# Kernel optimization log

Hardware: AMD Instinct MI355X
Metric: run time of the kernel (lower is better)

## Reference

```python
import math
import jax, jax.numpy as jnp
import numpy as np

NH, NKV, HD = 16, 8, 128  # n_heads, n_kv_heads, head_dim from config

def setup_inputs() -> dict:
    key = jax.random.key(0)
    ks = jax.random.split(key, 5)
    B, T, D = 2, 2048, 2048
    KV = NKV * HD  # 1024
    s = 1.0 / math.sqrt(D)
    return {
        "x": jax.random.normal(ks[0], (B, T, D), dtype=jnp.float32),
        "Wq": jax.random.normal(ks[1], (D, D), dtype=jnp.float32) * s,
        "Wk": jax.random.normal(ks[2], (KV, D), dtype=jnp.float32) * s,
        "Wv": jax.random.normal(ks[3], (KV, D), dtype=jnp.float32) * s,
        "Wo": jax.random.normal(ks[4], (D, D), dtype=jnp.float32) * s,
    }

def reference(x, Wq, Wk, Wv, Wo):
    B, T, D = x.shape
    groups = NH // NKV
    scale = 1.0 / math.sqrt(HD)
    # Projections (torch Linear: y = x @ W.T)
    q = (x @ Wq.T).reshape(B, T, NH, HD).transpose(0, 2, 1, 3)    # [B, nh, T, hd]
    k = (x @ Wk.T).reshape(B, T, NKV, HD).transpose(0, 2, 1, 3)   # [B, nkv, T, hd]
    v = (x @ Wv.T).reshape(B, T, NKV, HD).transpose(0, 2, 1, 3)   # [B, nkv, T, hd]
    kv_state = jnp.concatenate([k, v], axis=-1)                    # [B, nkv, T, 2*hd]
    # GQA: replicate kv heads (repeat_interleave along head dim)
    k = jnp.repeat(k, groups, axis=1)                              # [B, nh, T, hd]
    v = jnp.repeat(v, groups, axis=1)
    scores = jnp.einsum('bhqd,bhkd->bhqk', q, k) * scale           # [B, nh, T, T]
    causal = jnp.tril(jnp.ones((T, T), dtype=bool))
    scores = jnp.where(causal, scores, jnp.finfo(scores.dtype).min)
    probs = jax.nn.softmax(scores, axis=-1)
    attn = jnp.einsum('bhqk,bhkd->bhqd', probs, v)                 # [B, nh, T, hd]
    attn = attn.transpose(0, 2, 1, 3).reshape(B, T, NH * HD)
    output = attn @ Wo.T
    return (output, kv_state)
```

## Files before the change

### kernel.cpp

```cpp
#include <hip/hip_runtime.h>
#include <hip/hip_bf16.h>
#include <cstdint>
#include <cstddef>

#define DEV __device__ __forceinline__

typedef __attribute__((ext_vector_type(8))) short short8;
typedef __attribute__((ext_vector_type(4))) float f32x4;
typedef __attribute__((ext_vector_type(8))) __bf16 bf16x8;

DEV unsigned short f2bf(float f) {
    unsigned u = __builtin_bit_cast(unsigned, f);
    u += 0x7fffu + ((u >> 16) & 1u);
    return (unsigned short)(u >> 16);
}

DEV unsigned short f2bf_hw(float f) {
    return __builtin_bit_cast(unsigned short, (__bf16)f);
}

DEV f32x4 mfma16(short8 a, short8 b, f32x4 c) {
    return __builtin_amdgcn_mfma_f32_16x16x32_bf16(
        __builtin_bit_cast(bf16x8, a), __builtin_bit_cast(bf16x8, b), c, 0, 0, 0);
}

#define GLD_TO_LDS16(g, l)                                                  \
    __builtin_amdgcn_global_load_lds(                                       \
        (const __attribute__((address_space(1))) void*)(g),                 \
        (__attribute__((address_space(3))) void*)(l), 16, 0, 0)

__global__ void cvt_all(const float* __restrict__ x,  const float* __restrict__ wq,
                        const float* __restrict__ wk, const float* __restrict__ wv,
                        const float* __restrict__ wo,
                        unsigned short* __restrict__ xb,  unsigned short* __restrict__ wqb,
                        unsigned short* __restrict__ wkb, unsigned short* __restrict__ wvb,
                        unsigned short* __restrict__ wob) {
    constexpr int NX = 1048576, NQ = 524288, NK = 262144, NV = 262144, NO = 524288;
    constexpr int C1 = NX, C2 = C1 + NQ, C3 = C2 + NK, C4 = C3 + NV, C5 = C4 + NO;
    int i = blockIdx.x * blockDim.x + threadIdx.x;
    int stride = gridDim.x * blockDim.x;
    for (; i < C5; i += stride) {
        const float* s;
        unsigned short* d;
        int j;
        if (i < C1)      { s = x;  d = xb;  j = i; }
        else if (i < C2) { s = wq; d = wqb; j = i - C1; }
        else if (i < C3) { s = wk; d = wkb; j = i - C2; }
        else if (i < C4) { s = wv; d = wvb; j = i - C3; }
        else             { s = wo; d = wob; j = i - C4; }
        const f32x4* sp = (const f32x4*)(s + (size_t)j * 8);
        f32x4 a = sp[0], bq = sp[1];
        short8 o;
        o[0] = (short)f2bf(a[0]);  o[1] = (short)f2bf(a[1]);
        o[2] = (short)f2bf(a[2]);  o[3] = (short)f2bf(a[3]);
        o[4] = (short)f2bf(bq[0]); o[5] = (short)f2bf(bq[1]);
        o[6] = (short)f2bf(bq[2]); o[7] = (short)f2bf(bq[3]);
        *(short8*)(d + (size_t)j * 8) = o;
    }
}

__global__ __launch_bounds__(256) void transpose_v(
    const unsigned short* __restrict__ src, unsigned short* __restrict__ dst) {
    __shared__ __align__(16) unsigned short tile[64 * 64];
    const int t0 = blockIdx.x * 64;
    const int d0 = blockIdx.y * 64;
    const int b  = blockIdx.z;
    const int tid = threadIdx.x;
#pragma unroll
    for (int p = 0; p < 2; ++p) {
        int ch = tid + p * 256;
        int it = ch >> 3, ic8 = ch & 7;
        short8 v = *(const short8*)(src + (size_t)(b * 2048 + t0 + it) * 1024 + d0 + ic8 * 8);
        *(short8*)&tile[it * 64 + ((ic8 ^ (it & 7)) << 3)] = v;
    }
    __syncthreads();
#pragma unroll
    for (int p = 0; p < 2; ++p) {
        int ch = tid + p * 256;
        int od = ch >> 3, ot8 = ch & 7;
        short8 v;
#pragma unroll
        for (int j = 0; j < 8; ++j) {
            int t = ot8 * 8 + j;
            v[j] = (short)tile[t * 64 + ((((od >> 3) ^ (t & 7)) << 3) | (od & 7))];
        }
        *(short8*)(dst + (size_t)(b * 1024 + d0 + od) * 2048 + t0 + ot8 * 8) = v;
    }
}

__global__ __launch_bounds__(512, 2) void gemm_qkv_8p(
    const unsigned short* __restrict__ A,
    const unsigned short* __restrict__ Wq, const unsigned short* __restrict__ Wk,
    const unsigned short* __restrict__ Wv,
    unsigned short* __restrict__ Qo, unsigned short* __restrict__ Ko,
    unsigned short* __restrict__ Vo, float* __restrict__ kvf) {
    constexpr int K = 2048, BM = 256, KT = K / 64;
    __shared__ __align__(16) unsigned short sA[2][2][BM][32];
    __shared__ __align__(16) unsigned short sB[2][2][BM][32];

    const int tid = threadIdx.x, lane = tid & 63, w = tid >> 6;
    const int wm = w >> 2, wn = w & 3;
    const int lrow = lane & 15, lg = lane >> 4;
    const int m0 = blockIdx.y * BM, n0 = blockIdx.x * BM;

    const unsigned short* Bp;
    unsigned short* Co;
    int c0, ostr, doff = 0;
    bool iskv = false;
    if (n0 < 2048)      { Bp = Wq + (size_t)n0 * K;        Co = Qo; c0 = n0;        ostr = 2048; }
    else if (n0 < 3072) { Bp = Wk + (size_t)(n0-2048) * K; Co = Ko; c0 = n0 - 2048; ostr = 1024; iskv = true; }
    else                { Bp = Wv + (size_t)(n0-3072) * K; Co = Vo; c0 = n0 - 3072; ostr = 1024; iskv = true; doff = 128; }

    const unsigned short* Ab = A + (size_t)m0 * K;

    auto stage = [&](const unsigned short* gcol, unsigned short* lds) {
#pragma unroll
        for (int p = 0; p < 2; ++p) {
            int ch = tid + p * 512;
            int row = ch >> 2;
            int slot = (ch & 3) ^ (row & 3);
            GLD_TO_LDS16(gcol + (size_t)row * K + slot * 8, lds + ch * 8);
        }
    };

    f32x4 acc[8][4];
#pragma unroll
    for (int i = 0; i < 8; ++i)
#pragma unroll
        for (int j = 0; j < 4; ++j) acc[i][j] = (f32x4)0.f;

    const int xoff = (lg * 8) ^ ((lrow & 3) << 3);
    const int arow0 = wm * 128 + lrow;
    const int brow0 = wn * 64 + lrow;

    stage(Ab,      &sA[0][0][0][0]);
    stage(Bp,      &sB[0][0][0][0]);
    stage(Ab + 32, &sA[0][1][0][0]);
    stage(Bp + 32, &sB[0][1][0][0]);
    asm volatile("s_waitcnt vmcnt(4)\n\ts_barrier" ::: "memory");

    for (int kt = 0; kt < KT; ++kt) {
        const int buf = kt & 1, nb = buf ^ 1;
        const bool pre = (kt + 1 < KT);
        const unsigned short* An = Ab + (kt + 1) * 64;
        const unsigned short* Bn = Bp + (kt + 1) * 64;
        short8 bfrag[4], afrag[4];

        if (pre) stage(An, &sA[nb][0][0][0]);
#pragma unroll
        for (int ni = 0; ni < 4; ++ni)
            bfrag[ni] = *(const short8*)(&sB[buf][0][brow0 + ni * 16][0] + xoff);
#pragma unroll
        for (int mi = 0; mi < 4; ++mi)
            afrag[mi] = *(const short8*)(&sA[buf][0][arow0 + mi * 16][0] + xoff);
        __builtin_amdgcn_s_setprio(1);
#pragma unroll
        for (int mi = 0; mi < 4; ++mi)
#pragma unroll
            for (int ni = 0; ni < 4; ++ni)
                acc[mi][ni] = mfma16(afrag[mi], bfrag[ni], acc[mi][ni]);
        __builtin_amdgcn_s_setprio(0);

        if (pre) stage(Bn, &sB[nb][0][0][0]);
#pragma unroll
        for (int mi = 0; mi < 4; ++mi)
            afrag[mi] = *(const short8*)(&sA[buf][0][arow0 + 64 + mi * 16][0] + xoff);
        __builtin_amdgcn_s_setprio(1);
#pragma unroll
        for (int mi = 0; mi < 4; ++mi)
#pragma unroll
            for (int ni = 0; ni < 4; ++ni)
                acc[4 + mi][ni] = mfma16(afrag[mi], bfrag[ni], acc[4 + mi][ni]);
        __builtin_amdgcn_s_setprio(0);

        if (pre) asm volatile("s_waitcnt vmcnt(4)\n\ts_barrier" ::: "memory");
        else     asm volatile("s_waitcnt vmcnt(0)\n\ts_barrier" ::: "memory");

        if (pre) stage(An + 32, &sA[nb][1][0][0]);
#pragma unroll
        for (int ni = 0; ni < 4; ++ni)
            bfrag[ni] = *(const short8*)(&sB[buf][1][brow0 + ni * 16][0] + xoff);
#pragma unroll
        for (int mi = 0; mi < 4; ++mi)
            afrag[mi] = *(const short8*)(&sA[buf][1][arow0 + mi * 16][0] + xoff);
        __builtin_amdgcn_s_setprio(1);
#pragma unroll
        for (int mi = 0; mi < 4; ++mi)
#pragma unroll
            for (int ni = 0; ni < 4; ++ni)
                acc[mi][ni] = mfma16(afrag[mi], bfrag[ni], acc[mi][ni]);
        __builtin_amdgcn_s_setprio(0);

        if (pre) stage(Bn + 32, &sB[nb][1][0][0]);
#pragma unroll
        for (int mi = 0; mi < 4; ++mi)
            afrag[mi] = *(const short8*)(&sA[buf][1][arow0 + 64 + mi * 16][0] + xoff);
        __builtin_amdgcn_s_setprio(1);
#pragma unroll
        for (int mi = 0; mi < 4; ++mi)
#pragma unroll
            for (int ni = 0; ni < 4; ++ni)
                acc[4 + mi][ni] = mfma16(afrag[mi], bfrag[ni], acc[4 + mi][ni]);
        __builtin_amdgcn_s_setprio(0);

        if (pre) asm volatile("s_waitcnt vmcnt(4)\n\ts_barrier" ::: "memory");
    }

    const int lrow4 = (lane >> 4) * 4, lcol = lane & 15;
#pragma unroll
    for (int mi = 0; mi < 8; ++mi) {
#pragma unroll
        for (int ni = 0; ni < 4; ++ni) {
#pragma unroll
            for (int r = 0; r < 4; ++r) {
                int row = m0 + wm * 128 + mi * 16 + lrow4 + r;
                int col = c0 + wn * 64 + ni * 16 + lcol;
                float v = acc[mi][ni][r];
                Co[(size_t)row * ostr + col] = f2bf(v);
                if (iskv) {
                    int b = row >> 11, t = row & 2047;
                    int kh = col >> 7, d = col & 127;
                    kvf[((size_t)(b * 8 + kh) * 2048 + t) * 256 + doff + d] = v;
                }
            }
        }
    }
}

__global__ __launch_bounds__(512, 2) void gemm_o_2p(
    const unsigned short* __restrict__ A, const unsigned short* __restrict__ Bm,
    float* __restrict__ Cf) {
    constexpr int K = 2048, N = 2048, KT = K / 64;
    __shared__ __align__(16) unsigned short sA[2][2][256][32];
    __shared__ __align__(16) unsigned short sB[2][2][128][32];

    const int tid = threadIdx.x, lane = tid & 63, w = tid >> 6;
    const int wm = w >> 1, wn = w & 1;
    const int lrow = lane & 15, lg = lane >> 4;
    const int m0 = blockIdx.y * 256, n0 = blockIdx.x * 128;

    const unsigned short* Ab = A + (size_t)m0 * K;
    const unsigned short* Bb = Bm + (size_t)n0 * K;

    auto stageA = [&](const unsigned short* gcol, unsigned short* lds) {
#pragma unroll
        for (int p = 0; p < 2; ++p) {
            int ch = tid + p * 512;
            int row = ch >> 2;
            int slot = (ch & 3) ^ (row & 3);
            GLD_TO_LDS16(gcol + (size_t)row * K + slot * 8, lds + ch * 8);
        }
    };
    auto stageB = [&](const unsigned short* gcol, unsigned short* lds) {
        int ch = tid;
        int row = ch >> 2;
        int slot = (ch & 3) ^ (row & 3);
        GLD_TO_LDS16(gcol + (size_t)row * K + slot * 8, lds + ch * 8);
    };

    f32x4 acc[4][4];
#pragma unroll
    for (int i = 0; i < 4; ++i)
#pragma unroll
        for (int j = 0; j < 4; ++j) acc[i][j] = (f32x4)0.f;

    const int xoff = (lg * 8) ^ ((lrow & 3) << 3);
    const int arow0 = wm * 64 + lrow;
    const int brow0 = wn * 64 + lrow;

    stageA(Ab,      &sA[0][0][0][0]);
    stageB(Bb,      &sB[0][0][0][0]);
    stageA(Ab + 32, &sA[0][1][0][0]);
    stageB(Bb + 32, &sB[0][1][0][0]);
    asm volatile("s_waitcnt vmcnt(3)\n\ts_barrier" ::: "memory");

    for (int kt = 0; kt < KT; ++kt) {
        const int buf = kt & 1, nb = buf ^ 1;
        const bool pre = (kt + 1 < KT);
        const unsigned short* An = Ab + (kt + 1) * 64;
        const unsigned short* Bn = Bb + (kt + 1) * 64;
        short8 afrag[4], bfrag[4];

        if (pre) { stageA(An, &sA[nb][0][0][0]); stageB(Bn, &sB[nb][0][0][0]); }
#pragma unroll
        for (int ni = 0; ni < 4; ++ni)
            bfrag[ni] = *(const short8*)(&sB[buf][0][brow0 + ni * 16][0] + xoff);
#pragma unroll
        for (int mi = 0; mi < 4; ++mi)
            afrag[mi] = *(const short8*)(&sA[buf][0][arow0 + mi * 16][0] + xoff);
        __builtin_amdgcn_s_setprio(1);
#pragma unroll
        for (int mi = 0; mi < 4; ++mi)
#pragma unroll
            for (int ni = 0; ni < 4; ++ni)
                acc[mi][ni] = mfma16(afrag[mi], bfrag[ni], acc[mi][ni]);
        __builtin_amdgcn_s_setprio(0);

        if (pre) asm volatile("s_waitcnt vmcnt(3)\n\ts_barrier" ::: "memory");
        else     asm volatile("s_waitcnt vmcnt(0)\n\ts_barrier" ::: "memory");

        if (pre) { stageA(An + 32, &sA[nb][1][0][0]); stageB(Bn + 32, &sB[nb][1][0][0]); }
#pragma unroll
        for (int ni = 0; ni < 4; ++ni)
            bfrag[ni] = *(const short8*)(&sB[buf][1][brow0 + ni * 16][0] + xoff);
#pragma unroll
        for (int mi = 0; mi < 4; ++mi)
            afrag[mi] = *(const short8*)(&sA[buf][1][arow0 + mi * 16][0] + xoff);
        __builtin_amdgcn_s_setprio(1);
#pragma unroll
        for (int mi = 0; mi < 4; ++mi)
#pragma unroll
            for (int ni = 0; ni < 4; ++ni)
                acc[mi][ni] = mfma16(afrag[mi], bfrag[ni], acc[mi][ni]);
        __builtin_amdgcn_s_setprio(0);

        if (pre) asm volatile("s_waitcnt vmcnt(3)\n\ts_barrier" ::: "memory");
    }

    const int lrow4 = (lane >> 4) * 4, lcol = lane & 15;
#pragma unroll
    for (int mi = 0; mi < 4; ++mi)
#pragma unroll
        for (int ni = 0; ni < 4; ++ni)
#pragma unroll
            for (int r = 0; r < 4; ++r) {
                int row = m0 + wm * 64 + mi * 16 + lrow4 + r;
                int col = n0 + wn * 64 + ni * 16 + lcol;
                Cf[(size_t)row * N + col] = acc[mi][ni][r];
            }
}

__global__ __launch_bounds__(512, 2) void attn_fwd(
    const unsigned short* __restrict__ Qb, const unsigned short* __restrict__ Kb,
    const unsigned short* __restrict__ Vtg, unsigned short* __restrict__ Ob) {
    constexpr int T = 2048, DQ = 2048, DKV = 1024, HD = 128;
    constexpr float SC2 = 0.08838834764831845f * 1.4426950408889634f;
    constexpr float SHIFT = 8.0f * 1.4426950408889634f;
    __shared__ __align__(16) unsigned short Ks[2][64][128];
    __shared__ __align__(16) unsigned short Vs[2][128][64];
    __shared__ __align__(16) unsigned short Ps[8][16][64];

    const int bx = blockIdx.x, kh = blockIdx.y, b = blockIdx.z;
    const int qtile = b ? (31 - bx) : bx;
    const int tid = threadIdx.x, lane = tid & 63, w = tid >> 6;
    const int h = kh * 2 + (w >> 2);
    const int lrow = lane & 15, lg = lane >> 4;
    const int qt0 = qtile * 64;
    const int qrow0 = qt0 + (w & 3) * 16;
    const size_t bT = (size_t)b * T;

    short8 qf[4];
    {
        const unsigned short* qbase = Qb + (bT + qrow0 + lrow) * DQ + h * HD + lg * 8;
#pragma unroll
        for (int kc = 0; kc < 4; ++kc) qf[kc] = *(const short8*)(qbase + kc * 32);
    }

    int kr[2], kc8[2], vd[2], vk8[2];
#pragma unroll
    for (int p = 0; p < 2; ++p) {
        int ch = tid + p * 512;
        kr[p] = ch >> 4;  kc8[p] = ch & 15;
        vd[p] = ch >> 3;  vk8[p] = ch & 7;
    }
    const unsigned short* kbase = Kb + bT * DKV + kh * HD;
    const unsigned short* vbase = Vtg + (size_t)(b * 8 + kh) * 128 * T;
    short8 kreg[2], vreg[2];
    auto gload = [&](int kt) {
#pragma unroll
        for (int p = 0; p < 2; ++p) {
            kreg[p] = *(const short8*)(kbase + (size_t)(kt * 64 + kr[p]) * DKV + kc8[p] * 8);
            vreg[p] = *(const short8*)(vbase + (size_t)vd[p] * T + kt * 64 + vk8[p] * 8);
        }
    };
    auto lwrite = [&](int buf) {
#pragma unroll
        for (int p = 0; p < 2; ++p) {
            *(short8*)&Ks[buf][kr[p]][(kc8[p] ^ (kr[p] & 15)) << 3] = kreg[p];
            *(short8*)&Vs[buf][vd[p]][(vk8[p] ^ (vd[p] & 7)) << 3] = vreg[p];
        }
    };

    f32x4 o[8];
#pragma unroll
    for (int i = 0; i < 8; ++i) o[i] = (f32x4)0.f;
    float rsum[4] = {0.f, 0.f, 0.f, 0.f};

    const int nkt = qtile + 1;
    gload(0);
    for (int kt = 0; kt < nkt; ++kt) {
        const int kt0 = kt * 64;
        const int buf = kt & 1;
        lwrite(buf);
        __syncthreads();
        if (kt + 1 < nkt) gload(kt + 1);

        f32x4 s[4];
        __builtin_amdgcn_s_setprio(1);
#pragma unroll
        for (int nt = 0; nt < 4; ++nt) {
            s[nt] = (f32x4)0.f;
#pragma unroll
            for (int kc = 0; kc < 4; ++kc) {
                short8 kf = *(const short8*)&Ks[buf][nt * 16 + lrow][((kc * 4 + lg) ^ lrow) << 3];
                s[nt] = mfma16(qf[kc], kf, s[nt]);
            }
        }
        __builtin_amdgcn_s_setprio(0);

        const int qabs = qrow0 + lg * 4;
        const bool diag = (kt == qtile);
#pragma unroll
        for (int nt = 0; nt < 4; ++nt) {
            int kcol = kt0 + nt * 16 + lrow;
#pragma unroll
            for (int r = 0; r < 4; ++r) {
                float p = exp2f(fmaf(s[nt][r], SC2, -SHIFT));
                if (diag && kcol > qabs + r) p = 0.f;
                rsum[r] += p;
                int q = lg * 4 + r;
                Ps[w][q][((((nt * 2) + (lrow >> 3)) ^ (q & 7)) << 3) | (lrow & 7)] = f2bf_hw(p);
            }
        }

        __builtin_amdgcn_s_setprio(1);
#pragma unroll
        for (int kc2 = 0; kc2 < 2; ++kc2) {
            short8 pf = *(const short8*)&Ps[w][lrow][((kc2 * 4 + lg) ^ (lrow & 7)) << 3];
#pragma unroll
            for (int dt = 0; dt < 8; ++dt) {
                int d = dt * 16 + lrow;
                short8 vf = *(const short8*)&Vs[buf][d][((kc2 * 4 + lg) ^ (d & 7)) << 3];
                o[dt] = mfma16(pf, vf, o[dt]);
            }
        }
        __builtin_amdgcn_s_setprio(0);
    }

#pragma unroll
    for (int r = 0; r < 4; ++r) {
        float v = rsum[r];
        v += __shfl_xor(v, 1);
        v += __shfl_xor(v, 2);
        v += __shfl_xor(v, 4);
        v += __shfl_xor(v, 8);
        float inv = 1.f / v;
        int row = qrow0 + lg * 4 + r;
        unsigned short* obase = Ob + (bT + row) * DQ + h * HD + lrow;
#pragma unroll
        for (int dt = 0; dt < 8; ++dt) obase[dt * 16] = f2bf_hw(o[dt][r] * inv);
    }
}

extern "C" void kernel_launch(void* const* d_in, const int* in_sizes, int n_in,
                              void* d_out, int out_size, void* d_ws, size_t ws_size,
                              hipStream_t stream) {
    (void)in_sizes; (void)n_in; (void)out_size; (void)ws_size;
    const float* x  = (const float*)d_in[0];
    const float* Wq = (const float*)d_in[1];
    const float* Wk = (const float*)d_in[2];
    const float* Wv = (const float*)d_in[3];
    const float* Wo = (const float*)d_in[4];
    float* out = (float*)d_out;
    float* kv_out = out + (size_t)8388608;

    unsigned short* xb   = (unsigned short*)d_ws;
    unsigned short* wqb  = xb   + 8388608;
    unsigned short* wkb  = wqb  + 4194304;
    unsigned short* wvb  = wkb  + 2097152;
    unsigned short* wob  = wvb  + 2097152;
    unsigned short* qb   = wob  + 4194304;
    unsigned short* kb   = qb   + 8388608;
    unsigned short* vt   = kb   + 4194304;
    unsigned short* ab   = vt   + 4194304;
    unsigned short* vtmp = ab;

    cvt_all<<<dim3(2048), dim3(256), 0, stream>>>(x, Wq, Wk, Wv, Wo,
                                                  xb, wqb, wkb, wvb, wob);
    gemm_qkv_8p<<<dim3(16, 16), 512, 0, stream>>>(xb, wqb, wkb, wvb, qb, kb, vtmp, kv_out);
    transpose_v<<<dim3(32, 16, 2), 256, 0, stream>>>(vtmp, vt);
    attn_fwd<<<dim3(32, 8, 2), 512, 0, stream>>>(qb, kb, vt, ab);
    gemm_o_2p<<<dim3(16, 16), 512, 0, stream>>>(ab, wob, out);
}
```

Baseline: 252.1 us.

## Rework LDS swizzles in GEMMs, switch attention to padded single-buffer LDS

Changes the XOR swizzle in both GEMM kernels to use row>>1 bits, and switches the QKV epilogue to hardware bf16 conversion. The attention kernel drops its double-buffered, XOR-swizzled K/V/P shared memory in favour of single-buffered padded rows (stride 136/72) and adds an extra barrier before each LDS write. Its launch bound rises to 4 blocks per CU to gain occupancy from the smaller LDS footprint. The extra barrier and the register cap that comes with the higher occupancy target could stall or spill.

```diff
diff --git a/kernel.cpp b/kernel.cpp
--- a/kernel.cpp
+++ b/kernel.cpp
@@ -118,7 +118,7 @@
         for (int p = 0; p < 2; ++p) {
             int ch = tid + p * 512;
             int row = ch >> 2;
-            int slot = (ch & 3) ^ (row & 3);
+            int slot = (ch & 3) ^ ((row >> 1) & 3);
             GLD_TO_LDS16(gcol + (size_t)row * K + slot * 8, lds + ch * 8);
         }
     };
@@ -129,9 +129,9 @@
 #pragma unroll
         for (int j = 0; j < 4; ++j) acc[i][j] = (f32x4)0.f;
 
-    const int xoff = (lg * 8) ^ ((lrow & 3) << 3);
     const int arow0 = wm * 128 + lrow;
     const int brow0 = wn * 64 + lrow;
+    auto xr = [&](int row) { return (lg ^ ((row >> 1) & 3)) << 3; };
 
     stage(Ab,      &sA[0][0][0][0]);
     stage(Bp,      &sB[0][0][0][0]);
@@ -149,10 +149,10 @@
         if (pre) stage(An, &sA[nb][0][0][0]);
 #pragma unroll
         for (int ni = 0; ni < 4; ++ni)
-            bfrag[ni] = *(const short8*)(&sB[buf][0][brow0 + ni * 16][0] + xoff);
-#pragma unroll
-        for (int mi = 0; mi < 4; ++mi)
-            afrag[mi] = *(const short8*)(&sA[buf][0][arow0 + mi * 16][0] + xoff);
+            bfrag[ni] = *(const short8*)(&sB[buf][0][brow0 + ni * 16][0] + xr(brow0 + ni * 16));
+#pragma unroll
+        for (int mi = 0; mi < 4; ++mi)
+            afrag[mi] = *(const short8*)(&sA[buf][0][arow0 + mi * 16][0] + xr(arow0 + mi * 16));
         __builtin_amdgcn_s_setprio(1);
 #pragma unroll
         for (int mi = 0; mi < 4; ++mi)
@@ -164,7 +164,7 @@
         if (pre) stage(Bn, &sB[nb][0][0][0]);
 #pragma unroll
         for (int mi = 0; mi < 4; ++mi)
-            afrag[mi] = *(const short8*)(&sA[buf][0][arow0 + 64 + mi * 16][0] + xoff);
+            afrag[mi] = *(const short8*)(&sA[buf][0][arow0 + 64 + mi * 16][0] + xr(arow0 + 64 + mi * 16));
         __builtin_amdgcn_s_setprio(1);
 #pragma unroll
         for (int mi = 0; mi < 4; ++mi)
@@ -179,10 +179,10 @@
         if (pre) stage(An + 32, &sA[nb][1][0][0]);
 #pragma unroll
         for (int ni = 0; ni < 4; ++ni)
-            bfrag[ni] = *(const short8*)(&sB[buf][1][brow0 + ni * 16][0] + xoff);
-#pragma unroll
-        for (int mi = 0; mi < 4; ++mi)
-            afrag[mi] = *(const short8*)(&sA[buf][1][arow0 + mi * 16][0] + xoff);
+            bfrag[ni] = *(const short8*)(&sB[buf][1][brow0 + ni * 16][0] + xr(brow0 + ni * 16));
+#pragma unroll
+        for (int mi = 0; mi < 4; ++mi)
+            afrag[mi] = *(const short8*)(&sA[buf][1][arow0 + mi * 16][0] + xr(arow0 + mi * 16));
         __builtin_amdgcn_s_setprio(1);
 #pragma unroll
         for (int mi = 0; mi < 4; ++mi)
@@ -194,7 +194,7 @@
         if (pre) stage(Bn + 32, &sB[nb][1][0][0]);
 #pragma unroll
         for (int mi = 0; mi < 4; ++mi)
-            afrag[mi] = *(const short8*)(&sA[buf][1][arow0 + 64 + mi * 16][0] + xoff);
+            afrag[mi] = *(const short8*)(&sA[buf][1][arow0 + 64 + mi * 16][0] + xr(arow0 + 64 + mi * 16));
         __builtin_amdgcn_s_setprio(1);
 #pragma unroll
         for (int mi = 0; mi < 4; ++mi)
@@ -216,7 +216,7 @@
                 int row = m0 + wm * 128 + mi * 16 + lrow4 + r;
                 int col = c0 + wn * 64 + ni * 16 + lcol;
                 float v = acc[mi][ni][r];
-                Co[(size_t)row * ostr + col] = f2bf(v);
+                Co[(size_t)row * ostr + col] = f2bf_hw(v);
                 if (iskv) {
                     int b = row >> 11, t = row & 2047;
                     int kh = col >> 7, d = col & 127;
@@ -247,14 +247,14 @@
         for (int p = 0; p < 2; ++p) {
             int ch = tid + p * 512;
             int row = ch >> 2;
-            int slot = (ch & 3) ^ (row & 3);
+            int slot = (ch & 3) ^ ((row >> 1) & 3);
             GLD_TO_LDS16(gcol + (size_t)row * K + slot * 8, lds + ch * 8);
         }
     };
     auto stageB = [&](const unsigned short* gcol, unsigned short* lds) {
         int ch = tid;
         int row = ch >> 2;
-        int slot = (ch & 3) ^ (row & 3);
+        int slot = (ch & 3) ^ ((row >> 1) & 3);
         GLD_TO_LDS16(gcol + (size_t)row * K + slot * 8, lds + ch * 8);
     };
 
@@ -264,9 +264,9 @@
 #pragma unroll
         for (int j = 0; j < 4; ++j) acc[i][j] = (f32x4)0.f;
 
-    const int xoff = (lg * 8) ^ ((lrow & 3) << 3);
     const int arow0 = wm * 64 + lrow;
     const int brow0 = wn * 64 + lrow;
+    auto xr = [&](int row) { return (lg ^ ((row >> 1) & 3)) << 3; };
 
     stageA(Ab,      &sA[0][0][0][0]);
     stageB(Bb,      &sB[0][0][0][0]);
@@ -284,10 +284,10 @@
         if (pre) { stageA(An, &sA[nb][0][0][0]); stageB(Bn, &sB[nb][0][0][0]); }
 #pragma unroll
         for (int ni = 0; ni < 4; ++ni)
-            bfrag[ni] = *(const short8*)(&sB[buf][0][brow0 + ni * 16][0] + xoff);
-#pragma unroll
-        for (int mi = 0; mi < 4; ++mi)
-            afrag[mi] = *(const short8*)(&sA[buf][0][arow0 + mi * 16][0] + xoff);
+            bfrag[ni] = *(const short8*)(&sB[buf][0][brow0 + ni * 16][0] + xr(brow0 + ni * 16));
+#pragma unroll
+        for (int mi = 0; mi < 4; ++mi)
+            afrag[mi] = *(const short8*)(&sA[buf][0][arow0 + mi * 16][0] + xr(arow0 + mi * 16));
         __builtin_amdgcn_s_setprio(1);
 #pragma unroll
         for (int mi = 0; mi < 4; ++mi)
@@ -302,10 +302,10 @@
         if (pre) { stageA(An + 32, &sA[nb][1][0][0]); stageB(Bn + 32, &sB[nb][1][0][0]); }
 #pragma unroll
         for (int ni = 0; ni < 4; ++ni)
-            bfrag[ni] = *(const short8*)(&sB[buf][1][brow0 + ni * 16][0] + xoff);
-#pragma unroll
-        for (int mi = 0; mi < 4; ++mi)
-            afrag[mi] = *(const short8*)(&sA[buf][1][arow0 + mi * 16][0] + xoff);
+            bfrag[ni] = *(const short8*)(&sB[buf][1][brow0 + ni * 16][0] + xr(brow0 + ni * 16));
+#pragma unroll
+        for (int mi = 0; mi < 4; ++mi)
+            afrag[mi] = *(const short8*)(&sA[buf][1][arow0 + mi * 16][0] + xr(arow0 + mi * 16));
         __builtin_amdgcn_s_setprio(1);
 #pragma unroll
         for (int mi = 0; mi < 4; ++mi)
@@ -330,15 +330,15 @@
             }
 }
 
-__global__ __launch_bounds__(512, 2) void attn_fwd(
+__global__ __launch_bounds__(512, 4) void attn_fwd(
     const unsigned short* __restrict__ Qb, const unsigned short* __restrict__ Kb,
     const unsigned short* __restrict__ Vtg, unsigned short* __restrict__ Ob) {
     constexpr int T = 2048, DQ = 2048, DKV = 1024, HD = 128;
     constexpr float SC2 = 0.08838834764831845f * 1.4426950408889634f;
     constexpr float SHIFT = 8.0f * 1.4426950408889634f;
-    __shared__ __align__(16) unsigned short Ks[2][64][128];
-    __shared__ __align__(16) unsigned short Vs[2][128][64];
-    __shared__ __align__(16) unsigned short Ps[8][16][64];
+    __shared__ __align__(16) unsigned short Ks[64 * 136];
+    __shared__ __align__(16) unsigned short Vs[128 * 72];
+    __shared__ __align__(16) unsigned short Ps[8][16 * 72];
 
     const int bx = blockIdx.x, kh = blockIdx.y, b = blockIdx.z;
     const int qtile = b ? (31 - bx) : bx;
@@ -373,11 +373,11 @@
             vreg[p] = *(const short8*)(vbase + (size_t)vd[p] * T + kt * 64 + vk8[p] * 8);
         }
     };
-    auto lwrite = [&](int buf) {
+    auto lwrite = [&]() {
 #pragma unroll
         for (int p = 0; p < 2; ++p) {
-            *(short8*)&Ks[buf][kr[p]][(kc8[p] ^ (kr[p] & 15)) << 3] = kreg[p];
-            *(short8*)&Vs[buf][vd[p]][(vk8[p] ^ (vd[p] & 7)) << 3] = vreg[p];
+            *(short8*)&Ks[kr[p] * 136 + kc8[p] * 8] = kreg[p];
+            *(short8*)&Vs[vd[p] * 72 + vk8[p] * 8] = vreg[p];
         }
     };
 
@@ -390,8 +390,8 @@
     gload(0);
     for (int kt = 0; kt < nkt; ++kt) {
         const int kt0 = kt * 64;
-        const int buf = kt & 1;
-        lwrite(buf);
+        __syncthreads();
+        lwrite();
         __syncthreads();
         if (kt + 1 < nkt) gload(kt + 1);
 
@@ -402,7 +402,7 @@
             s[nt] = (f32x4)0.f;
 #pragma unroll
             for (int kc = 0; kc < 4; ++kc) {
-                short8 kf = *(const short8*)&Ks[buf][nt * 16 + lrow][((kc * 4 + lg) ^ lrow) << 3];
+                short8 kf = *(const short8*)&Ks[(nt * 16 + lrow) * 136 + kc * 32 + lg * 8];
                 s[nt] = mfma16(qf[kc], kf, s[nt]);
             }
         }
@@ -418,19 +418,17 @@
                 float p = exp2f(fmaf(s[nt][r], SC2, -SHIFT));
                 if (diag && kcol > qabs + r) p = 0.f;
                 rsum[r] += p;
-                int q = lg * 4 + r;
-                Ps[w][q][((((nt * 2) + (lrow >> 3)) ^ (q & 7)) << 3) | (lrow & 7)] = f2bf_hw(p);
+                Ps[w][(lg * 4 + r) * 72 + nt * 16 + lrow] = f2bf_hw(p);
             }
         }
 
         __builtin_amdgcn_s_setprio(1);
 #pragma unroll
         for (int kc2 = 0; kc2 < 2; ++kc2) {
-            short8 pf = *(const short8*)&Ps[w][lrow][((kc2 * 4 + lg) ^ (lrow & 7)) << 3];
+            short8 pf = *(const short8*)&Ps[w][lrow * 72 + kc2 * 32 + lg * 8];
 #pragma unroll
             for (int dt = 0; dt < 8; ++dt) {
-                int d = dt * 16 + lrow;
-                short8 vf = *(const short8*)&Vs[buf][d][((kc2 * 4 + lg) ^ (d & 7)) << 3];
+                short8 vf = *(const short8*)&Vs[(dt * 16 + lrow) * 72 + kc2 * 32 + lg * 8];
                 o[dt] = mfma16(pf, vf, o[dt]);
             }
         }
```

Result: faster. 237.5 us (-5.8%).
